# Kernel tuning notes

Hardware: AMD Instinct MI355X
Metric: run time of the kernel (lower is better)

## Reference

```python
import jax, jax.numpy as jnp
import numpy as np

ALPHA = 40.0
BETA = 20.0
NUM_INSTANCES = 8  # samples per class in the PK-sampled batch


def setup_inputs() -> dict:
    key = jax.random.key(0)
    n, d = 4096, 1024
    x = jax.random.normal(key, (n, d), dtype=jnp.float32)
    # L2-normalize embeddings (standard for this loss; margins 0.8/1.1 assume dist in [0,2])
    inputs = x / jnp.linalg.norm(x, axis=1, keepdims=True)
    targets = (jnp.arange(n) // NUM_INSTANCES).astype(jnp.int32)
    return {"inputs": inputs, "targets": targets}


def reference(inputs, targets):
    n = inputs.shape[0]
    # euclidean_dist: ||xi||^2 + ||xj||^2 - 2 xi.xj, clamp, sqrt
    sq = jnp.sum(inputs * inputs, axis=1)  # [n]
    dist = sq[:, None] + sq[None, :] - 2.0 * (inputs @ inputs.T)
    dist = jnp.sqrt(jnp.clip(dist, 1e-12, None))  # [n, n]

    same = targets[:, None] == targets[None, :]
    eye = jnp.eye(n, dtype=bool)
    pos_mask = same & ~eye   # positives excluding self
    neg_mask = ~same         # negatives

    exp_a = jnp.exp(ALPHA * (1.0 - dist))
    pos_logit = jnp.sum(jnp.where(pos_mask, exp_a, 0.0), axis=1)  # [n]
    neg_logit = jnp.sum(jnp.where(neg_mask, exp_a, 0.0), axis=1)  # [n]
    # a_lr is computed from .data in the original (detached)
    a_lr = jax.lax.stop_gradient(1.0 - pos_logit / (pos_logit + neg_logit))

    pos_loss = jnp.log(jnp.sum(jnp.where(pos_mask, jnp.exp(BETA * (dist - 0.8)), 0.0), axis=1))
    neg_loss = jnp.log(jnp.sum(jnp.where(neg_mask, jnp.exp(BETA * (1.1 - dist)), 0.0), axis=1))
    loss = jnp.mean(a_lr * (pos_loss + neg_loss))

    # acc_num never incremented in the original -> accuracy == 0
    accuracy = jnp.zeros((), dtype=jnp.float32)
    pos_d = jax.lax.stop_gradient(
        jnp.sum(jnp.where(pos_mask, dist, 0.0)) / jnp.sum(pos_mask))
    neg_d = jax.lax.stop_gradient(
        jnp.sum(jnp.where(neg_mask, dist, 0.0)) / jnp.sum(neg_mask))
    return jnp.stack([loss, accuracy, pos_d, neg_d])  # [4]
```

## Files before the change

### kernel.cpp

```cpp
#include <hip/hip_runtime.h>

#define N 4096
#define D 1024
#define BM 128
#define BN 128
#define BK 32
#define NSLOT 32

typedef __bf16 bf16x8 __attribute__((ext_vector_type(8)));
typedef float floatx4 __attribute__((ext_vector_type(4)));

__device__ __forceinline__ ushort f2bf(float f) {
    union { float f; uint32_t u; } c; c.f = f;
    uint32_t u = c.u;
    uint32_t r = u + 0x7FFFu + ((u >> 16) & 1u);
    return (ushort)(r >> 16);
}

__global__ __launch_bounds__(256) void prep_kernel(const float* __restrict__ x,
                                                   ushort* __restrict__ xb,
                                                   float* __restrict__ sq) {
    int row = blockIdx.x;
    int tid = threadIdx.x;
    float4 v = ((const float4*)(x + (size_t)row * D))[tid];
    float s = v.x * v.x + v.y * v.y + v.z * v.z + v.w * v.w;
    ushort4 b = make_ushort4(f2bf(v.x), f2bf(v.y), f2bf(v.z), f2bf(v.w));
    ((ushort4*)(xb + (size_t)row * D))[tid] = b;

    #pragma unroll
    for (int sh = 1; sh < 64; sh <<= 1) s += __shfl_xor(s, sh);
    __shared__ float wsum[4];
    int lane = tid & 63, w = tid >> 6;
    if (lane == 0) wsum[w] = s;
    __syncthreads();
    if (tid == 0) sq[row] = wsum[0] + wsum[1] + wsum[2] + wsum[3];
}

__global__ __launch_bounds__(256, 2) void gemm_fused(const ushort* __restrict__ xb,
                                                     const float* __restrict__ sq,
                                                     float* __restrict__ colPart) {
    __shared__ ushort smem[2 * BM * BK];

    const int bi = blockIdx.y, bj = blockIdx.x;
    const int i0 = bi * BM, j0 = bj * BN;
    const int tid = threadIdx.x;
    const int lane = tid & 63, wave = tid >> 6;
    const int wm = wave >> 1, wn = wave & 1;
    const int quad = lane >> 4, c16 = lane & 15;

    floatx4 acc[4][4];
    #pragma unroll
    for (int a = 0; a < 4; ++a)
        #pragma unroll
        for (int b = 0; b < 4; ++b) acc[a][b] = (floatx4){0.f, 0.f, 0.f, 0.f};

    for (int kt = 0; kt < D; kt += BK) {
        #pragma unroll
        for (int it = 0; it < 4; ++it) {
            int chunk = it * 256 + tid;
            int half = chunk >> 9;
            int c = chunk & 511;
            int row = c >> 2, kc = c & 3;
            int grow = (half ? j0 : i0) + row;
            const ushort* gp = xb + (size_t)grow * D + kt + kc * 8;
            ushort* lp = smem + chunk * 8;
            __builtin_amdgcn_global_load_lds(
                (const __attribute__((address_space(1))) void*)gp,
                (__attribute__((address_space(3))) void*)lp, 16, 0, 0);
        }
        __syncthreads();

        bf16x8 afrag[4], bfrag[4];
        #pragma unroll
        for (int t = 0; t < 4; ++t) {
            afrag[t] = *(const bf16x8*)(smem + ((wm * 64 + t * 16 + c16) * BK + quad * 8));
            bfrag[t] = *(const bf16x8*)(smem + BM * BK + ((wn * 64 + t * 16 + c16) * BK + quad * 8));
        }
        #pragma unroll
        for (int tm = 0; tm < 4; ++tm)
            #pragma unroll
            for (int tn = 0; tn < 4; ++tn)
                acc[tm][tn] = __builtin_amdgcn_mfma_f32_16x16x32_bf16(
                    afrag[tm], bfrag[tn], acc[tm][tn], 0, 0, 0);
        __syncthreads();
    }

    float sqi[4][4];
    #pragma unroll
    for (int tm = 0; tm < 4; ++tm)
        #pragma unroll
        for (int r = 0; r < 4; ++r)
            sqi[tm][r] = sq[i0 + wm * 64 + tm * 16 + quad * 4 + r];
    float sqj[4];
    #pragma unroll
    for (int tn = 0; tn < 4; ++tn)
        sqj[tn] = sq[j0 + wn * 64 + tn * 16 + c16];

    float cpa[4], cna[4], cpb[4], cnb[4], cpd[4], cnd[4];
    const bool diag = (bi == bj);

    #pragma unroll
    for (int tn = 0; tn < 4; ++tn) {
        float pa = 0.f, na = 0.f, pb = 0.f, nb = 0.f, pd = 0.f, nd = 0.f;
        if (!diag) {
            #pragma unroll
            for (int tm = 0; tm < 4; ++tm)
                #pragma unroll
                for (int r = 0; r < 4; ++r) {
                    float dot = acc[tm][tn][r];
                    float dsq = sqi[tm][r] + sqj[tn] - 2.0f * dot;
                    float dist = sqrtf(fmaxf(dsq, 1e-12f));
                    float t = __expf(20.0f * (1.1f - dist));
                    na = fmaf(t, t, na);
                    nb += t;
                    nd += dist;
                }
        } else {
            const int gjc = (j0 + wn * 64 + tn * 16 + c16) >> 3;
            const int gj = j0 + wn * 64 + tn * 16 + c16;
            #pragma unroll
            for (int tm = 0; tm < 4; ++tm)
                #pragma unroll
                for (int r = 0; r < 4; ++r) {
                    const int gi = i0 + wm * 64 + tm * 16 + quad * 4 + r;
                    float dot = acc[tm][tn][r];
                    float dsq = sqi[tm][r] + sqj[tn] - 2.0f * dot;
                    float dist = sqrtf(fmaxf(dsq, 1e-12f));
                    float t = __expf(20.0f * (1.1f - dist));
                    bool same = (gi >> 3) == gjc;
                    if (same) {
                        if (gi != gj) {
                            pa = fmaf(t, t, pa);
                            pb += __expf(20.0f * (dist - 0.8f));
                            pd += dist;
                        }
                    } else {
                        na = fmaf(t, t, na);
                        nb += t;
                        nd += dist;
                    }
                }
        }
        cpa[tn] = pa; cna[tn] = na; cpb[tn] = pb;
        cnb[tn] = nb; cpd[tn] = pd; cnd[tn] = nd;
    }

    #pragma unroll
    for (int tn = 0; tn < 4; ++tn) {
        #pragma unroll
        for (int s = 16; s < 64; s <<= 1) {
            cna[tn] += __shfl_xor(cna[tn], s);
            cnb[tn] += __shfl_xor(cnb[tn], s);
            cnd[tn] += __shfl_xor(cnd[tn], s);
        }
        if (diag) {
            #pragma unroll
            for (int s = 16; s < 64; s <<= 1) {
                cpa[tn] += __shfl_xor(cpa[tn], s);
                cpb[tn] += __shfl_xor(cpb[tn], s);
                cpd[tn] += __shfl_xor(cpd[tn], s);
            }
        }
    }

    float* colBuf = (float*)smem;
    #pragma unroll
    for (int tn = 0; tn < 4; ++tn) {
        int cb = (wm * 128 + wn * 64 + tn * 16 + c16) * 6;
        colBuf[cb + 0] = cpa[tn]; colBuf[cb + 1] = cna[tn];
        colBuf[cb + 2] = cpb[tn]; colBuf[cb + 3] = cnb[tn];
        colBuf[cb + 4] = cpd[tn]; colBuf[cb + 5] = cnd[tn];
    }
    __syncthreads();

    float* dst = colPart + (size_t)bi * N * 6 + (size_t)j0 * 6;
    #pragma unroll
    for (int it = 0; it < 3; ++it) {
        int idx = it * 256 + tid;
        dst[idx] = colBuf[idx] + colBuf[768 + idx];
    }
}

__global__ __launch_bounds__(256) void reduce_rows(const float* __restrict__ colPart,
                                                   float* __restrict__ rowOut) {
    int j = blockIdx.x * 256 + threadIdx.x;
    float pa = 0.f, na = 0.f, pb = 0.f, nb = 0.f, pd = 0.f, nd = 0.f;
    for (int s = 0; s < NSLOT; ++s) {
        const float* p = colPart + (size_t)s * N * 6 + (size_t)j * 6;
        pa += p[0]; na += p[1]; pb += p[2];
        nb += p[3]; pd += p[4]; nd += p[5];
    }
    float a_lr = 1.0f - pa / (pa + na);
    rowOut[j * 3 + 0] = a_lr * (logf(pb) + logf(nb));
    rowOut[j * 3 + 1] = pd;
    rowOut[j * 3 + 2] = nd;
}

__global__ __launch_bounds__(256) void finalize_kernel(const float* __restrict__ rowOut,
                                                       float* __restrict__ out) {
    int tid = threadIdx.x;
    float L = 0.f, P = 0.f, G = 0.f;
    for (int i = tid; i < N; i += 256) {
        L += rowOut[i * 3 + 0];
        P += rowOut[i * 3 + 1];
        G += rowOut[i * 3 + 2];
    }
    #pragma unroll
    for (int s = 1; s < 64; s <<= 1) {
        L += __shfl_xor(L, s);
        P += __shfl_xor(P, s);
        G += __shfl_xor(G, s);
    }
    __shared__ float r0[4], r1[4], r2[4];
    int lane = tid & 63, w = tid >> 6;
    if (lane == 0) { r0[w] = L; r1[w] = P; r2[w] = G; }
    __syncthreads();
    if (tid == 0) {
        float Ls = r0[0] + r0[1] + r0[2] + r0[3];
        float Ps = r1[0] + r1[1] + r1[2] + r1[3];
        float Gs = r2[0] + r2[1] + r2[2] + r2[3];
        out[0] = Ls / (float)N;
        out[1] = 0.0f;
        out[2] = Ps / ((float)N * 7.0f);
        out[3] = Gs / ((float)N * (float)(N - 8));
    }
}

extern "C" void kernel_launch(void* const* d_in, const int* in_sizes, int n_in,
                              void* d_out, int out_size, void* d_ws, size_t ws_size,
                              hipStream_t stream) {
    const float* x = (const float*)d_in[0];
    float* out = (float*)d_out;
    char* ws = (char*)d_ws;

    ushort* xb      = (ushort*)ws;
    float*  sq      = (float*)(ws + (size_t)N * D * 2);
    float*  colPart = (float*)(ws + (size_t)N * D * 2 + N * 4);
    float*  rowOut  = (float*)(ws + (size_t)N * D * 2 + N * 4
                               + (size_t)NSLOT * N * 6 * 4);

    prep_kernel<<<N, 256, 0, stream>>>(x, xb, sq);

    dim3 grid(N / BN, N / BM);
    gemm_fused<<<grid, 256, 0, stream>>>(xb, sq, colPart);

    reduce_rows<<<N / 256, 256, 0, stream>>>(colPart, rowOut);
    finalize_kernel<<<1, 256, 0, stream>>>(rowOut, out);
}
```

Baseline: 122.5 us.

## Exploit distance symmetry: compute only upper-triangular tiles, emit row and column partials

The distance matrix is symmetric, so the GEMM grid is cut to the 528 lower-triangular tile pairs. Each off-diagonal tile writes its column partials and also its row partials, reduced by 16-lane shuffles, into the transposed slot of the partial buffer. The LDS staging layout is also changed so each MFMA fragment load is a contiguous 16-byte-per-lane read, and the prep kernel now processes four rows per block with one wave per row and no shared-memory reduction. This roughly halves the matmul and exp work, at the cost of extra per-row accumulators, more register pressure and an uneven load between diagonal and off-diagonal blocks.

```diff
diff --git a/kernel.cpp b/kernel.cpp
--- a/kernel.cpp
+++ b/kernel.cpp
@@ -6,6 +6,7 @@
 #define BN 128
 #define BK 32
 #define NSLOT 32
+#define NTRI 528
 
 typedef __bf16 bf16x8 __attribute__((ext_vector_type(8)));
 typedef float floatx4 __attribute__((ext_vector_type(4)));
@@ -20,20 +21,20 @@
 __global__ __launch_bounds__(256) void prep_kernel(const float* __restrict__ x,
                                                    ushort* __restrict__ xb,
                                                    float* __restrict__ sq) {
-    int row = blockIdx.x;
-    int tid = threadIdx.x;
-    float4 v = ((const float4*)(x + (size_t)row * D))[tid];
-    float s = v.x * v.x + v.y * v.y + v.z * v.z + v.w * v.w;
-    ushort4 b = make_ushort4(f2bf(v.x), f2bf(v.y), f2bf(v.z), f2bf(v.w));
-    ((ushort4*)(xb + (size_t)row * D))[tid] = b;
-
+    int row = blockIdx.x * 4 + (threadIdx.x >> 6);
+    int lane = threadIdx.x & 63;
+    const float4* xr = (const float4*)(x + (size_t)row * D);
+    ushort4* br = (ushort4*)(xb + (size_t)row * D);
+    float s = 0.f;
+    #pragma unroll
+    for (int j = 0; j < 4; ++j) {
+        float4 v = xr[j * 64 + lane];
+        s += v.x * v.x + v.y * v.y + v.z * v.z + v.w * v.w;
+        br[j * 64 + lane] = make_ushort4(f2bf(v.x), f2bf(v.y), f2bf(v.z), f2bf(v.w));
+    }
     #pragma unroll
     for (int sh = 1; sh < 64; sh <<= 1) s += __shfl_xor(s, sh);
-    __shared__ float wsum[4];
-    int lane = tid & 63, w = tid >> 6;
-    if (lane == 0) wsum[w] = s;
-    __syncthreads();
-    if (tid == 0) sq[row] = wsum[0] + wsum[1] + wsum[2] + wsum[3];
+    if (lane == 0) sq[row] = s;
 }
 
 __global__ __launch_bounds__(256, 2) void gemm_fused(const ushort* __restrict__ xb,
@@ -41,13 +42,30 @@
                                                      float* __restrict__ colPart) {
     __shared__ ushort smem[2 * BM * BK];
 
-    const int bi = blockIdx.y, bj = blockIdx.x;
+    int kblk = blockIdx.x;
+    int bi = (int)((sqrtf(8.0f * kblk + 1.0f) - 1.0f) * 0.5f);
+    if ((bi + 1) * (bi + 2) / 2 <= kblk) bi++;
+    if (bi * (bi + 1) / 2 > kblk) bi--;
+    int bj = kblk - bi * (bi + 1) / 2;
+
     const int i0 = bi * BM, j0 = bj * BN;
     const int tid = threadIdx.x;
     const int lane = tid & 63, wave = tid >> 6;
     const int wm = wave >> 1, wn = wave & 1;
     const int quad = lane >> 4, c16 = lane & 15;
 
+    int s_half[4], s_row[4], s_kc[4];
+    #pragma unroll
+    for (int it = 0; it < 4; ++it) {
+        int chunk = it * 256 + tid;
+        int half = chunk >> 9;
+        int c = chunk & 511;
+        int g = c >> 6, p = c & 63;
+        s_half[it] = half;
+        s_kc[it] = p >> 4;
+        s_row[it] = g * 16 + (p & 15);
+    }
+
     floatx4 acc[4][4];
     #pragma unroll
     for (int a = 0; a < 4; ++a)
@@ -57,13 +75,9 @@
     for (int kt = 0; kt < D; kt += BK) {
         #pragma unroll
         for (int it = 0; it < 4; ++it) {
-            int chunk = it * 256 + tid;
-            int half = chunk >> 9;
-            int c = chunk & 511;
-            int row = c >> 2, kc = c & 3;
-            int grow = (half ? j0 : i0) + row;
-            const ushort* gp = xb + (size_t)grow * D + kt + kc * 8;
-            ushort* lp = smem + chunk * 8;
+            int grow = (s_half[it] ? j0 : i0) + s_row[it];
+            const ushort* gp = xb + (size_t)grow * D + kt + s_kc[it] * 8;
+            ushort* lp = smem + (it * 256 + tid) * 8;
             __builtin_amdgcn_global_load_lds(
                 (const __attribute__((address_space(1))) void*)gp,
                 (__attribute__((address_space(3))) void*)lp, 16, 0, 0);
@@ -73,8 +87,8 @@
         bf16x8 afrag[4], bfrag[4];
         #pragma unroll
         for (int t = 0; t < 4; ++t) {
-            afrag[t] = *(const bf16x8*)(smem + ((wm * 64 + t * 16 + c16) * BK + quad * 8));
-            bfrag[t] = *(const bf16x8*)(smem + BM * BK + ((wn * 64 + t * 16 + c16) * BK + quad * 8));
+            afrag[t] = *(const bf16x8*)(smem + (wm * 4 + t) * 512 + lane * 8);
+            bfrag[t] = *(const bf16x8*)(smem + 4096 + (wn * 4 + t) * 512 + lane * 8);
         }
         #pragma unroll
         for (int tm = 0; tm < 4; ++tm)
@@ -96,13 +110,20 @@
     for (int tn = 0; tn < 4; ++tn)
         sqj[tn] = sq[j0 + wn * 64 + tn * 16 + c16];
 
-    float cpa[4], cna[4], cpb[4], cnb[4], cpd[4], cnd[4];
+    float* colBuf = (float*)smem;
+    float* rowBuf = colBuf + 1536;
     const bool diag = (bi == bj);
 
-    #pragma unroll
-    for (int tn = 0; tn < 4; ++tn) {
-        float pa = 0.f, na = 0.f, pb = 0.f, nb = 0.f, pd = 0.f, nd = 0.f;
-        if (!diag) {
+    if (!diag) {
+        float rna[4][4], rnb[4][4], rnd[4][4];
+        #pragma unroll
+        for (int tm = 0; tm < 4; ++tm)
+            #pragma unroll
+            for (int r = 0; r < 4; ++r) { rna[tm][r] = 0.f; rnb[tm][r] = 0.f; rnd[tm][r] = 0.f; }
+
+        #pragma unroll
+        for (int tn = 0; tn < 4; ++tn) {
+            float na = 0.f, nb = 0.f, nd = 0.f;
             #pragma unroll
             for (int tm = 0; tm < 4; ++tm)
                 #pragma unroll
@@ -114,10 +135,41 @@
                     na = fmaf(t, t, na);
                     nb += t;
                     nd += dist;
-                }
-        } else {
-            const int gjc = (j0 + wn * 64 + tn * 16 + c16) >> 3;
+                    rna[tm][r] = fmaf(t, t, rna[tm][r]);
+                    rnb[tm][r] += t;
+                    rnd[tm][r] += dist;
+                }
+            #pragma unroll
+            for (int s = 16; s < 64; s <<= 1) {
+                na += __shfl_xor(na, s); nb += __shfl_xor(nb, s); nd += __shfl_xor(nd, s);
+            }
+            int cb = (wm * 128 + wn * 64 + tn * 16 + c16) * 6;
+            colBuf[cb + 0] = 0.f; colBuf[cb + 1] = na;
+            colBuf[cb + 2] = 0.f; colBuf[cb + 3] = nb;
+            colBuf[cb + 4] = 0.f; colBuf[cb + 5] = nd;
+        }
+        #pragma unroll
+        for (int tm = 0; tm < 4; ++tm)
+            #pragma unroll
+            for (int r = 0; r < 4; ++r) {
+                float a = rna[tm][r], b = rnb[tm][r], d = rnd[tm][r];
+                #pragma unroll
+                for (int s = 1; s < 16; s <<= 1) {
+                    a += __shfl_xor(a, s); b += __shfl_xor(b, s); d += __shfl_xor(d, s);
+                }
+                if (c16 == 0) {
+                    int rb = (wn * 128 + wm * 64 + tm * 16 + quad * 4 + r) * 6;
+                    rowBuf[rb + 0] = 0.f; rowBuf[rb + 1] = a;
+                    rowBuf[rb + 2] = 0.f; rowBuf[rb + 3] = b;
+                    rowBuf[rb + 4] = 0.f; rowBuf[rb + 5] = d;
+                }
+            }
+    } else {
+        #pragma unroll
+        for (int tn = 0; tn < 4; ++tn) {
             const int gj = j0 + wn * 64 + tn * 16 + c16;
+            const int gjc = gj >> 3;
+            float pa = 0.f, na = 0.f, pb = 0.f, nb = 0.f, pd = 0.f, nd = 0.f;
             #pragma unroll
             for (int tm = 0; tm < 4; ++tm)
                 #pragma unroll
@@ -140,44 +192,33 @@
                         nd += dist;
                     }
                 }
-        }
-        cpa[tn] = pa; cna[tn] = na; cpb[tn] = pb;
-        cnb[tn] = nb; cpd[tn] = pd; cnd[tn] = nd;
-    }
-
-    #pragma unroll
-    for (int tn = 0; tn < 4; ++tn) {
-        #pragma unroll
-        for (int s = 16; s < 64; s <<= 1) {
-            cna[tn] += __shfl_xor(cna[tn], s);
-            cnb[tn] += __shfl_xor(cnb[tn], s);
-            cnd[tn] += __shfl_xor(cnd[tn], s);
-        }
-        if (diag) {
             #pragma unroll
             for (int s = 16; s < 64; s <<= 1) {
-                cpa[tn] += __shfl_xor(cpa[tn], s);
-                cpb[tn] += __shfl_xor(cpb[tn], s);
-                cpd[tn] += __shfl_xor(cpd[tn], s);
+                pa += __shfl_xor(pa, s); na += __shfl_xor(na, s);
+                pb += __shfl_xor(pb, s); nb += __shfl_xor(nb, s);
+                pd += __shfl_xor(pd, s); nd += __shfl_xor(nd, s);
             }
-        }
-    }
-
-    float* colBuf = (float*)smem;
-    #pragma unroll
-    for (int tn = 0; tn < 4; ++tn) {
-        int cb = (wm * 128 + wn * 64 + tn * 16 + c16) * 6;
-        colBuf[cb + 0] = cpa[tn]; colBuf[cb + 1] = cna[tn];
-        colBuf[cb + 2] = cpb[tn]; colBuf[cb + 3] = cnb[tn];
-        colBuf[cb + 4] = cpd[tn]; colBuf[cb + 5] = cnd[tn];
+            int cb = (wm * 128 + wn * 64 + tn * 16 + c16) * 6;
+            colBuf[cb + 0] = pa; colBuf[cb + 1] = na;
+            colBuf[cb + 2] = pb; colBuf[cb + 3] = nb;
+            colBuf[cb + 4] = pd; colBuf[cb + 5] = nd;
+        }
     }
     __syncthreads();
 
-    float* dst = colPart + (size_t)bi * N * 6 + (size_t)j0 * 6;
+    float* dstC = colPart + ((size_t)bi * N + j0) * 6;
     #pragma unroll
     for (int it = 0; it < 3; ++it) {
         int idx = it * 256 + tid;
-        dst[idx] = colBuf[idx] + colBuf[768 + idx];
+        dstC[idx] = colBuf[idx] + colBuf[768 + idx];
+    }
+    if (!diag) {
+        float* dstR = colPart + ((size_t)bj * N + i0) * 6;
+        #pragma unroll
+        for (int it = 0; it < 3; ++it) {
+            int idx = it * 256 + tid;
+            dstR[idx] = rowBuf[idx] + rowBuf[768 + idx];
+        }
     }
 }
 
@@ -239,10 +280,9 @@
     float*  rowOut  = (float*)(ws + (size_t)N * D * 2 + N * 4
                                + (size_t)NSLOT * N * 6 * 4);
 
-    prep_kernel<<<N, 256, 0, stream>>>(x, xb, sq);
-
-    dim3 grid(N / BN, N / BM);
-    gemm_fused<<<grid, 256, 0, stream>>>(xb, sq, colPart);
+    prep_kernel<<<N / 4, 256, 0, stream>>>(x, xb, sq);
+
+    gemm_fused<<<NTRI, 256, 0, stream>>>(xb, sq, colPart);
 
     reduce_rows<<<N / 256, 256, 0, stream>>>(colPart, rowOut);
     finalize_kernel<<<1, 256, 0, stream>>>(rowOut, out);
```

After: 146.9 us. 19.9% more time.

## Reorder LDS tile layout for conflict-free MFMA loads and fuse reduction kernels

Applied to the files above, without the earlier changes.

The global-to-LDS copy now places each 16-row by 32-k fragment contiguously in lane order, so every MFMA operand read is a linear 16-byte-per-lane LDS access instead of a row-strided one. The global offsets for these loads are computed once, outside the k loop. The prep kernel handles four rows per block with one wave per row and no shared-memory reduction. The row-reduce and finalize kernels are merged, using atomicAdd into the output, which prep zeroes first. This removes one launch and the rowOut round trip, at the cost of nondeterministic float summation order.

```diff
diff --git a/kernel.cpp b/kernel.cpp
--- a/kernel.cpp
+++ b/kernel.cpp
@@ -19,21 +19,25 @@
 
 __global__ __launch_bounds__(256) void prep_kernel(const float* __restrict__ x,
                                                    ushort* __restrict__ xb,
-                                                   float* __restrict__ sq) {
-    int row = blockIdx.x;
-    int tid = threadIdx.x;
-    float4 v = ((const float4*)(x + (size_t)row * D))[tid];
-    float s = v.x * v.x + v.y * v.y + v.z * v.z + v.w * v.w;
-    ushort4 b = make_ushort4(f2bf(v.x), f2bf(v.y), f2bf(v.z), f2bf(v.w));
-    ((ushort4*)(xb + (size_t)row * D))[tid] = b;
-
+                                                   float* __restrict__ sq,
+                                                   float* __restrict__ out) {
+    if (blockIdx.x == 0 && threadIdx.x == 0) {
+        out[0] = 0.f; out[1] = 0.f; out[2] = 0.f; out[3] = 0.f;
+    }
+    int row = blockIdx.x * 4 + (threadIdx.x >> 6);
+    int lane = threadIdx.x & 63;
+    const float4* xr = (const float4*)(x + (size_t)row * D);
+    ushort4* br = (ushort4*)(xb + (size_t)row * D);
+    float s = 0.f;
+    #pragma unroll
+    for (int j = 0; j < 4; ++j) {
+        float4 v = xr[j * 64 + lane];
+        s += v.x * v.x + v.y * v.y + v.z * v.z + v.w * v.w;
+        br[j * 64 + lane] = make_ushort4(f2bf(v.x), f2bf(v.y), f2bf(v.z), f2bf(v.w));
+    }
     #pragma unroll
     for (int sh = 1; sh < 64; sh <<= 1) s += __shfl_xor(s, sh);
-    __shared__ float wsum[4];
-    int lane = tid & 63, w = tid >> 6;
-    if (lane == 0) wsum[w] = s;
-    __syncthreads();
-    if (tid == 0) sq[row] = wsum[0] + wsum[1] + wsum[2] + wsum[3];
+    if (lane == 0) sq[row] = s;
 }
 
 __global__ __launch_bounds__(256, 2) void gemm_fused(const ushort* __restrict__ xb,
@@ -48,6 +52,18 @@
     const int wm = wave >> 1, wn = wave & 1;
     const int quad = lane >> 4, c16 = lane & 15;
 
+    int goff[4];
+    #pragma unroll
+    for (int it = 0; it < 4; ++it) {
+        int chunk = it * 256 + tid;
+        int half = chunk >> 9;
+        int c = chunk & 511;
+        int g = c >> 6, p = c & 63;
+        int kc = p >> 4, r = p & 15;
+        int grow = (half ? j0 : i0) + g * 16 + r;
+        goff[it] = grow * D + kc * 8;
+    }
+
     floatx4 acc[4][4];
     #pragma unroll
     for (int a = 0; a < 4; ++a)
@@ -57,13 +73,8 @@
     for (int kt = 0; kt < D; kt += BK) {
         #pragma unroll
         for (int it = 0; it < 4; ++it) {
-            int chunk = it * 256 + tid;
-            int half = chunk >> 9;
-            int c = chunk & 511;
-            int row = c >> 2, kc = c & 3;
-            int grow = (half ? j0 : i0) + row;
-            const ushort* gp = xb + (size_t)grow * D + kt + kc * 8;
-            ushort* lp = smem + chunk * 8;
+            const ushort* gp = xb + goff[it] + kt;
+            ushort* lp = smem + (it * 256 + tid) * 8;
             __builtin_amdgcn_global_load_lds(
                 (const __attribute__((address_space(1))) void*)gp,
                 (__attribute__((address_space(3))) void*)lp, 16, 0, 0);
@@ -73,8 +84,8 @@
         bf16x8 afrag[4], bfrag[4];
         #pragma unroll
         for (int t = 0; t < 4; ++t) {
-            afrag[t] = *(const bf16x8*)(smem + ((wm * 64 + t * 16 + c16) * BK + quad * 8));
-            bfrag[t] = *(const bf16x8*)(smem + BM * BK + ((wn * 64 + t * 16 + c16) * BK + quad * 8));
+            afrag[t] = *(const bf16x8*)(smem + (wm * 4 + t) * 512 + lane * 8);
+            bfrag[t] = *(const bf16x8*)(smem + 4096 + (wn * 4 + t) * 512 + lane * 8);
         }
         #pragma unroll
         for (int tm = 0; tm < 4; ++tm)
@@ -116,8 +127,8 @@
                     nd += dist;
                 }
         } else {
-            const int gjc = (j0 + wn * 64 + tn * 16 + c16) >> 3;
             const int gj = j0 + wn * 64 + tn * 16 + c16;
+            const int gjc = gj >> 3;
             #pragma unroll
             for (int tm = 0; tm < 4; ++tm)
                 #pragma unroll
@@ -181,8 +192,8 @@
     }
 }
 
-__global__ __launch_bounds__(256) void reduce_rows(const float* __restrict__ colPart,
-                                                   float* __restrict__ rowOut) {
+__global__ __launch_bounds__(256) void reduce_finalize(const float* __restrict__ colPart,
+                                                       float* __restrict__ out) {
     int j = blockIdx.x * 256 + threadIdx.x;
     float pa = 0.f, na = 0.f, pb = 0.f, nb = 0.f, pd = 0.f, nd = 0.f;
     for (int s = 0; s < NSLOT; ++s) {
@@ -191,38 +202,25 @@
         nb += p[3]; pd += p[4]; nd += p[5];
     }
     float a_lr = 1.0f - pa / (pa + na);
-    rowOut[j * 3 + 0] = a_lr * (logf(pb) + logf(nb));
-    rowOut[j * 3 + 1] = pd;
-    rowOut[j * 3 + 2] = nd;
-}
-
-__global__ __launch_bounds__(256) void finalize_kernel(const float* __restrict__ rowOut,
-                                                       float* __restrict__ out) {
-    int tid = threadIdx.x;
-    float L = 0.f, P = 0.f, G = 0.f;
-    for (int i = tid; i < N; i += 256) {
-        L += rowOut[i * 3 + 0];
-        P += rowOut[i * 3 + 1];
-        G += rowOut[i * 3 + 2];
-    }
+    float L = a_lr * (logf(pb) + logf(nb));
+
     #pragma unroll
     for (int s = 1; s < 64; s <<= 1) {
-        L += __shfl_xor(L, s);
-        P += __shfl_xor(P, s);
-        G += __shfl_xor(G, s);
+        L  += __shfl_xor(L, s);
+        pd += __shfl_xor(pd, s);
+        nd += __shfl_xor(nd, s);
     }
     __shared__ float r0[4], r1[4], r2[4];
-    int lane = tid & 63, w = tid >> 6;
-    if (lane == 0) { r0[w] = L; r1[w] = P; r2[w] = G; }
+    int lane = threadIdx.x & 63, w = threadIdx.x >> 6;
+    if (lane == 0) { r0[w] = L; r1[w] = pd; r2[w] = nd; }
     __syncthreads();
-    if (tid == 0) {
+    if (threadIdx.x == 0) {
         float Ls = r0[0] + r0[1] + r0[2] + r0[3];
         float Ps = r1[0] + r1[1] + r1[2] + r1[3];
         float Gs = r2[0] + r2[1] + r2[2] + r2[3];
-        out[0] = Ls / (float)N;
-        out[1] = 0.0f;
-        out[2] = Ps / ((float)N * 7.0f);
-        out[3] = Gs / ((float)N * (float)(N - 8));
+        atomicAdd(out + 0, Ls / (float)N);
+        atomicAdd(out + 2, Ps / ((float)N * 7.0f));
+        atomicAdd(out + 3, Gs / ((float)N * (float)(N - 8)));
     }
 }
 
@@ -236,14 +234,11 @@
     ushort* xb      = (ushort*)ws;
     float*  sq      = (float*)(ws + (size_t)N * D * 2);
     float*  colPart = (float*)(ws + (size_t)N * D * 2 + N * 4);
-    float*  rowOut  = (float*)(ws + (size_t)N * D * 2 + N * 4
-                               + (size_t)NSLOT * N * 6 * 4);
-
-    prep_kernel<<<N, 256, 0, stream>>>(x, xb, sq);
+
+    prep_kernel<<<N / 4, 256, 0, stream>>>(x, xb, sq, out);
 
     dim3 grid(N / BN, N / BM);
     gemm_fused<<<grid, 256, 0, stream>>>(xb, sq, colPart);
 
-    reduce_rows<<<N / 256, 256, 0, stream>>>(colPart, rowOut);
-    finalize_kernel<<<1, 256, 0, stream>>>(rowOut, out);
-}
+    reduce_finalize<<<N / 256, 256, 0, stream>>>(colPart, out);
+}
```

Measured after the change: 140.7 us. 1.15x slower.
